# Optimization experiments

Hardware: AMD Instinct MI355X
Metric: run time of the kernel (lower is better)

## Reference

```python
import jax, jax.numpy as jnp
import numpy as np

# Config (mirrors init_kwargs)
B, S = 1, 2048          # batch, seq_len
H = 2048                # hidden_size
NH, NKV = 16, 8         # attention heads, kv heads (GQA n_rep = 2)
HD = H // NH            # head_dim = 128
I = 5632                # intermediate_size
L = 2                   # num_hidden_layers
V = 32000               # vocab_size
WIN = 1024              # sliding_window
THETA = 10000.0
EPS = 1e-6


def setup_inputs() -> dict:
    key = jax.random.key(0)
    ks = jax.random.split(key, 12)
    s = 0.02
    return {
        "input_ids": jax.random.randint(ks[0], (B, S), 0, V, dtype=jnp.int32),
        "embed": jax.random.normal(ks[1], (V, H), jnp.float32) * s,
        "Wq": jax.random.normal(ks[2], (L, H, NH * HD), jnp.float32) * s,
        "Wk": jax.random.normal(ks[3], (L, H, NKV * HD), jnp.float32) * s,
        "Wv": jax.random.normal(ks[4], (L, H, NKV * HD), jnp.float32) * s,
        "Wo": jax.random.normal(ks[5], (L, NH * HD, H), jnp.float32) * s,
        "Wg": jax.random.normal(ks[6], (L, H, I), jnp.float32) * s,
        "Wu": jax.random.normal(ks[7], (L, H, I), jnp.float32) * s,
        "Wd": jax.random.normal(ks[8], (L, I, H), jnp.float32) * s,
        "ln1": jnp.ones((L, H), jnp.float32),
        "ln2": jnp.ones((L, H), jnp.float32),
        "norm_w": jnp.ones((H,), jnp.float32),
    }


def _rmsnorm(x, w, eps=EPS):
    return x * jax.lax.rsqrt(jnp.mean(x * x, axis=-1, keepdims=True) + eps) * w


def _rope_tables(seq_len, dim, theta):
    inv_freq = 1.0 / (theta ** (jnp.arange(0, dim, 2, dtype=jnp.float32) / dim))
    freqs = jnp.arange(seq_len, dtype=jnp.float32)[:, None] * inv_freq[None, :]  # [S, dim/2]
    emb = jnp.concatenate([freqs, freqs], axis=-1)  # [S, dim]
    return jnp.cos(emb), jnp.sin(emb)


def _rotate_half(x):
    half = x.shape[-1] // 2
    return jnp.concatenate([-x[..., half:], x[..., :half]], axis=-1)


def _sliding_window_causal_mask(seq_len, window, dtype):
    i = jnp.arange(seq_len)[:, None]
    j = jnp.arange(seq_len)[None, :]
    allowed = (j <= i) & (j >= i - window)  # band: causal + sliding window
    return jnp.where(allowed, 0.0, jnp.finfo(dtype).min).astype(dtype)[None, None]  # [1,1,S,S]


def _forward(input_ids, embed, Wq, Wk, Wv, Wo, Wg, Wu, Wd, ln1, ln2, norm_w):
    x = embed[input_ids]  # [B,S,H]
    cos, sin = _rope_tables(S, HD, THETA)          # [S,HD]
    cos = cos[None, :, None, :]                    # [1,S,1,HD]
    sin = sin[None, :, None, :]
    mask = _sliding_window_causal_mask(S, WIN, x.dtype)  # [1,1,S,S]
    scale = 1.0 / jnp.sqrt(jnp.float32(HD)).astype(x.dtype)
    n_rep = NH // NKV

    for l in range(L):
        # --- attention block ---
        h = _rmsnorm(x, ln1[l])
        q = (h @ Wq[l]).reshape(B, S, NH, HD)
        k = (h @ Wk[l]).reshape(B, S, NKV, HD)
        v = (h @ Wv[l]).reshape(B, S, NKV, HD)
        q = q * cos + _rotate_half(q) * sin
        k = k * cos + _rotate_half(k) * sin
        # repeat_kv (GQA)
        k = jnp.broadcast_to(k[:, :, :, None, :], (B, S, NKV, n_rep, HD)).reshape(B, S, NH, HD)
        v = jnp.broadcast_to(v[:, :, :, None, :], (B, S, NKV, n_rep, HD)).reshape(B, S, NH, HD)
        scores = jnp.einsum('bshn,bthn->bhst', q, k) * scale + mask  # [B,NH,S,S]
        attn = jax.nn.softmax(scores.astype(jnp.float32), axis=-1).astype(x.dtype)
        o = jnp.einsum('bhst,bthn->bshn', attn, v).reshape(B, S, NH * HD)
        x = x + o @ Wo[l]
        # --- MLP block (SwiGLU) ---
        h = _rmsnorm(x, ln2[l])
        x = x + (jax.nn.silu(h @ Wg[l]) * (h @ Wu[l])) @ Wd[l]

    return _rmsnorm(x, norm_w)


def reference(input_ids, embed, Wq, Wk, Wv, Wo, Wg, Wu, Wd, ln1, ln2, norm_w):
    return _forward(input_ids, embed, Wq, Wk, Wv, Wo, Wg, Wu, Wd, ln1, ln2, norm_w)
```

## Files before the change

### kernel.cpp

```cpp
#include <hip/hip_runtime.h>
#include <stdint.h>

using bf16x8 = __attribute__((ext_vector_type(8))) __bf16;
using f32x4  = __attribute__((ext_vector_type(4))) float;

#define DEVI __device__ __forceinline__

DEVI unsigned short f2b(float f) {
  unsigned int u = __builtin_bit_cast(unsigned int, f);
  u = (u + 0x7FFFu + ((u >> 16) & 1u)) >> 16;
  return (unsigned short)u;
}
DEVI float b2f(unsigned short h) {
  unsigned int u = ((unsigned int)h) << 16;
  return __builtin_bit_cast(float, u);
}
DEVI f32x4 mfma16(bf16x8 a, bf16x8 b, f32x4 c) {
  return __builtin_amdgcn_mfma_f32_16x16x32_bf16(a, b, c, 0, 0, 0);
}
#define GLD(gp, lp) __builtin_amdgcn_global_load_lds( \
    (__attribute__((address_space(1))) void*)(uintptr_t)(gp), \
    (__attribute__((address_space(3))) void*)(uintptr_t)(lp), 16, 0, 0)

static constexpr int S_LEN = 2048;
static constexpr int HDIM  = 2048;
static constexpr int NH    = 16;
static constexpr int NKV   = 8;
static constexpr int HD    = 128;
static constexpr int IFF   = 5632;
static constexpr int WIN   = 1024;

DEVI void rms_finish(float4 v0, float4 v1, const float* __restrict__ w,
                     void* __restrict__ outp, int s, int t, int outf32) {
  float ss = v0.x*v0.x + v0.y*v0.y + v0.z*v0.z + v0.w*v0.w +
             v1.x*v1.x + v1.y*v1.y + v1.z*v1.z + v1.w*v1.w;
  #pragma unroll
  for (int off = 32; off >= 1; off >>= 1) ss += __shfl_xor(ss, off, 64);
  __shared__ float red[4];
  if ((t & 63) == 0) red[t >> 6] = ss;
  __syncthreads();
  ss = red[0] + red[1] + red[2] + red[3];
  float rr = rsqrtf(ss * (1.0f / 2048.0f) + 1e-6f);
  const float4* w4 = (const float4*)w;
  float4 w0 = w4[t], w1 = w4[t + 256];
  float o0x = v0.x*rr*w0.x, o0y = v0.y*rr*w0.y, o0z = v0.z*rr*w0.z, o0w = v0.w*rr*w0.w;
  float o1x = v1.x*rr*w1.x, o1y = v1.y*rr*w1.y, o1z = v1.z*rr*w1.z, o1w = v1.w*rr*w1.w;
  if (outf32) {
    float4* o4 = (float4*)outp + (size_t)s * 512;
    o4[t]       = make_float4(o0x, o0y, o0z, o0w);
    o4[t + 256] = make_float4(o1x, o1y, o1z, o1w);
  } else {
    uint2* ob = (uint2*)((unsigned short*)outp + (size_t)s * HDIM);
    ob[t]       = make_uint2((unsigned)f2b(o0x) | ((unsigned)f2b(o0y) << 16),
                             (unsigned)f2b(o0z) | ((unsigned)f2b(o0w) << 16));
    ob[t + 256] = make_uint2((unsigned)f2b(o1x) | ((unsigned)f2b(o1y) << 16),
                             (unsigned)f2b(o1z) | ((unsigned)f2b(o1w) << 16));
  }
}

__global__ __launch_bounds__(256) void gather_kernel(const int* __restrict__ ids,
    const float* __restrict__ embed, float* __restrict__ x,
    float* __restrict__ ct, float* __restrict__ st,
    const float* __restrict__ ln1w, unsigned short* __restrict__ h) {
  int s = blockIdx.x, t = threadIdx.x;
  const float4* src = (const float4*)(embed + (size_t)ids[s] * HDIM);
  float4* dst = (float4*)(x + (size_t)s * HDIM);
  float4 v0 = src[t], v1 = src[t + 256];
  dst[t]       = v0;
  dst[t + 256] = v1;
  if (t < 64) {
    float inv = expf(-(float)t * (9.210340371976184f / 64.0f));
    float f = (float)s * inv;
    ct[s * 64 + t] = cosf(f);
    st[s * 64 + t] = sinf(f);
  }
  rms_finish(v0, v1, ln1w, h, s, t, 0);
}

template<int OUTF32, int NPARTS>
__global__ __launch_bounds__(256) void rmsnorm_combine_kernel(
    float* __restrict__ x, const unsigned short* __restrict__ parts,
    const float* __restrict__ w, void* __restrict__ outp) {
  int s = blockIdx.x, t = threadIdx.x;
  const size_t PS = (size_t)2048 * 2048;
  float4* row = (float4*)(x + (size_t)s * HDIM);
  float4 v0 = row[t], v1 = row[t + 256];
  #pragma unroll
  for (int p = 0; p < NPARTS; ++p) {
    const unsigned short* pr = parts + p * PS + (size_t)s * HDIM;
    uint2 a = *(const uint2*)(pr + t * 4);
    uint2 b = *(const uint2*)(pr + (t + 256) * 4);
    v0.x += b2f((unsigned short)a.x); v0.y += b2f((unsigned short)(a.x >> 16));
    v0.z += b2f((unsigned short)a.y); v0.w += b2f((unsigned short)(a.y >> 16));
    v1.x += b2f((unsigned short)b.x); v1.y += b2f((unsigned short)(b.x >> 16));
    v1.z += b2f((unsigned short)b.y); v1.w += b2f((unsigned short)(b.y >> 16));
  }
  row[t] = v0; row[t + 256] = v1;
  rms_finish(v0, v1, w, outp, s, t, OUTF32);
}

__global__ __launch_bounds__(256) void convert_weights_kernel(
    const float* __restrict__ Wq, const float* __restrict__ Wk,
    const float* __restrict__ Wv, const float* __restrict__ Wo,
    const float* __restrict__ Wg, const float* __restrict__ Wu,
    const float* __restrict__ Wd,
    unsigned short* wqkvT, unsigned short* woT,
    unsigned short* wguT, unsigned short* wdT) {
  __shared__ float tl[128 * 65];
  int b = blockIdx.x;
  const float* in; unsigned short* out; int istr, ostr, tilesN, t; int guAdd = -1;
  if (b < 512)       { in = Wq; out = wqkvT;                       istr = 2048; ostr = 2048; tilesN = 32; t = b; }
  else if (b < 768)  { in = Wk; out = wqkvT + (size_t)2048 * 2048; istr = 1024; ostr = 2048; tilesN = 16; t = b - 512; }
  else if (b < 1024) { in = Wv; out = wqkvT + (size_t)3072 * 2048; istr = 1024; ostr = 2048; tilesN = 16; t = b - 768; }
  else if (b < 1536) { in = Wo; out = woT;                         istr = 2048; ostr = 2048; tilesN = 32; t = b - 1024; }
  else if (b < 2944) { in = Wg; out = wguT;                        istr = 5632; ostr = 2048; tilesN = 88; t = b - 1536; guAdd = 0; }
  else if (b < 4352) { in = Wu; out = wguT;                        istr = 5632; ostr = 2048; tilesN = 88; t = b - 2944; guAdd = 128; }
  else               { in = Wd; out = wdT;                         istr = 2048; ostr = 5632; tilesN = 32; t = b - 4352; }
  int k0 = (t / tilesN) * 128, n0 = (t % tilesN) * 64;
  int tx = threadIdx.x & 63, ty = threadIdx.x >> 6;
  #pragma unroll
  for (int i = 0; i < 32; ++i)
    tl[(ty + 4 * i) * 65 + tx] = in[(size_t)(k0 + ty + 4 * i) * istr + (n0 + tx)];
  __syncthreads();
  int ob = (guAdd >= 0) ? (((n0 >> 7) << 8) + (n0 & 64) + guAdd) : n0;
  unsigned int* ou = (unsigned int*)out;
  const int kstr2 = ostr >> 1;
  #pragma unroll
  for (int i = 0; i < 16; ++i) {
    int nrow = ty + 4 * i;
    float lo = tl[(2 * tx) * 65 + nrow], hi = tl[(2 * tx + 1) * 65 + nrow];
    ou[(size_t)(ob + nrow) * kstr2 + (k0 >> 1) + tx] =
        (unsigned int)f2b(lo) | ((unsigned int)f2b(hi) << 16);
  }
}

DEVI bf16x8 ldsAB(const unsigned short* buf, int r, int cbyte) {
  return *(const bf16x8*)((const unsigned char*)buf + r * 128 + (cbyte ^ ((r & 7) << 4)));
}
DEVI void stage_unit(const unsigned short* __restrict__ G, int Kstr,
                     unsigned short* lbuf, int loff0, int grow0,
                     int loff1, int grow1, int w, int l) {
  const int rsub = l >> 3;
  const int ce = ((l & 7) ^ rsub) << 3;
  const unsigned short* s0 = G + (size_t)(grow0 + w * 8 + rsub) * Kstr + ce;
  GLD(s0, (unsigned char*)lbuf + loff0 + w * 1024 + l * 16);
  const unsigned short* s1 = G + (size_t)(grow1 + w * 8 + rsub) * Kstr + ce;
  GLD(s1, (unsigned char*)lbuf + loff1 + w * 1024 + l * 16);
}
DEVI void stage128(const unsigned short* __restrict__ G, int Kstr,
                   unsigned short* slotbase, int h, int w, int l) {
  stage_unit(G, Kstr, slotbase, h * 16384, h * 128, h * 16384 + 8192, h * 128 + 64, w, l);
}

template<int Q>
DEVI void phase128(const unsigned short* Ab, f32x4 (&acc)[4][4],
                   bf16x8 (&breg)[2][4], int wr, int lg, int li) {
  const int r0 = wr * 64 + Q * 16 + li;
  bf16x8 a0 = ldsAB(Ab, r0, lg * 16);
  bf16x8 a1 = ldsAB(Ab, r0, 64 + lg * 16);
  __builtin_amdgcn_s_setprio(1);
  #pragma unroll
  for (int n = 0; n < 4; ++n) acc[Q][n] = mfma16(a0, breg[0][n], acc[Q][n]);
  #pragma unroll
  for (int n = 0; n < 4; ++n) acc[Q][n] = mfma16(a1, breg[1][n], acc[Q][n]);
  __builtin_amdgcn_s_setprio(0);
}

template<int EPI>
__global__ __launch_bounds__(512, 1) void gemm128_kernel(
    const unsigned short* __restrict__ A, const unsigned short* __restrict__ Bt,
    void* __restrict__ Cout, int Kstr, int nt, int parts, int nbm, int ldc,
    long long partStride,
    const float* __restrict__ ct, const float* __restrict__ st,
    unsigned short* __restrict__ ko, unsigned short* __restrict__ vt) {
  __shared__ __align__(16) unsigned char smem[131072];
  unsigned short* As0 = (unsigned short*)smem;
  unsigned short* Bs0 = (unsigned short*)(smem + 32768);
  const int tid = threadIdx.x, l = tid & 63, w = tid >> 6;
  const int lg = l >> 4, li = l & 15;
  const int wr = w >> 2, wc = w & 3;
  const int nb = gridDim.x, qx = nb >> 3;
  const int wg = ((int)blockIdx.x & 7) * qx + ((int)blockIdx.x >> 3);
  const int nbT = nb / parts;
  const int tile = wg % nbT, part = wg / nbT;
  const int m0 = (tile % nbm) * 128, n0 = (tile / nbm) * 256;
  const int kOff = part * (nt << 6);
  const unsigned short* At  = A  + (size_t)m0 * Kstr + kOff;
  const unsigned short* Bto = Bt + (size_t)n0 * Kstr + kOff;
  f32x4 acc[4][4] = {};
  bf16x8 breg[2][4];

  stage_unit(Bto, Kstr, Bs0, 0, 0, 8192, 64, w, l);
  stage_unit(Bto, Kstr, Bs0, 16384, 128, 24576, 192, w, l);
  stage_unit(At,  Kstr, As0, 0, 0, 8192, 64, w, l);
  { int k1 = (nt > 1) ? 64 : 0;
    stage_unit(Bto + k1, Kstr, Bs0 + 16384, 0, 0, 8192, 64, w, l);
    stage_unit(Bto + k1, Kstr, Bs0 + 16384, 16384, 128, 24576, 192, w, l); }
  asm volatile("s_waitcnt vmcnt(4)\n\ts_barrier" ::: "memory");

  for (int t = 0; t < nt; ++t) {
    unsigned short* Ab  = As0 + (t & 1) * 8192;
    unsigned short* Bb  = Bs0 + (t & 1) * 16384;
    unsigned short* Abn = As0 + ((t & 1) ^ 1) * 8192;
    const int kt1 = ((t + 1 < nt) ? t + 1 : nt - 1) << 6;
    const int kt2 = ((t + 2 < nt) ? t + 2 : nt - 1) << 6;
    stage_unit(At + kt1, Kstr, Abn, 0, 0, 8192, 64, w, l);
    #pragma unroll
    for (int ks = 0; ks < 2; ++ks)
      #pragma unroll
      for (int n = 0; n < 4; ++n)
        breg[ks][n] = ldsAB(Bb, wc * 64 + n * 16 + li, ks * 64 + lg * 16);
    asm volatile("s_waitcnt lgkmcnt(0)\n\ts_barrier" ::: "memory");
    phase128<0>(Ab, acc, breg, wr, lg, li);
    stage_unit(Bto + kt2, Kstr, Bb, 0, 0, 8192, 64, w, l);
    phase128<1>(Ab, acc, breg, wr, lg, li);
    stage_unit(Bto + kt2, Kstr, Bb, 16384, 128, 24576, 192, w, l);
    phase128<2>(Ab, acc, breg, wr, lg, li);
    phase128<3>(Ab, acc, breg, wr, lg, li);
    asm volatile("s_waitcnt vmcnt(4) lgkmcnt(0)\n\ts_barrier" ::: "memory");
  }
  asm volatile("s_waitcnt vmcnt(0)" ::: "memory");

  if (EPI == 0) {
    unsigned short* C = (unsigned short*)Cout + (size_t)part * (size_t)partStride;
    #pragma unroll
    for (int m = 0; m < 4; ++m)
      #pragma unroll
      for (int n = 0; n < 4; ++n) {
        int col = n0 + wc * 64 + n * 16 + li;
        #pragma unroll
        for (int r = 0; r < 4; ++r) {
          int row = m0 + wr * 64 + m * 16 + lg * 4 + r;
          C[(size_t)row * ldc + col] = f2b(acc[m][n][r]);
        }
      }
  } else {
    float* dump = (float*)smem;
    asm volatile("s_barrier" ::: "memory");
    #pragma unroll
    for (int m = 0; m < 4; ++m)
      #pragma unroll
      for (int n = 0; n < 4; ++n) {
        int colL = wc * 64 + n * 16 + li;
        #pragma unroll
        for (int r = 0; r < 4; ++r) {
          int rowl = wr * 64 + m * 16 + lg * 4 + r;
          dump[rowl * 256 + colL] = acc[m][n][r];
        }
      }
    asm volatile("s_waitcnt lgkmcnt(0)\n\ts_barrier" ::: "memory");
    if (n0 < 3072) {
      unsigned short* qk = (n0 < 2048) ? (unsigned short*)Cout : ko;
      const int cbase = (n0 < 2048) ? n0 : (n0 - 2048);
      const int ostr  = (n0 < 2048) ? 2048 : 1024;
      #pragma unroll
      for (int m = 0; m < 4; ++m)
        #pragma unroll
        for (int n = 0; n < 4; ++n) {
          int colL = wc * 64 + n * 16 + li;
          int hi = colL & 64;
          #pragma unroll
          for (int r = 0; r < 4; ++r) {
            int rowl = wr * 64 + m * 16 + lg * 4 + r;
            int s = m0 + rowl;
            float own = dump[rowl * 256 + colL];
            float par = dump[rowl * 256 + (colL ^ 64)];
            float c  = ct[s * 64 + (colL & 63)];
            float sn = st[s * 64 + (colL & 63)];
            float v = hi ? (own * c + par * sn) : (own * c - par * sn);
            qk[(size_t)s * ostr + cbase + colL] = f2b(v);
          }
        }
    } else {
      int vcol = tid >> 1, sh = (tid & 1) * 64;
      unsigned short* dstp = vt + (size_t)(n0 - 3072 + vcol) * 2048 + m0 + sh;
      #pragma unroll
      for (int c8 = 0; c8 < 8; ++c8) {
        unsigned short pk[8];
        #pragma unroll
        for (int i = 0; i < 8; ++i)
          pk[i] = f2b(dump[(sh + c8 * 8 + i) * 256 + vcol]);
        *(uint4*)(dstp + c8 * 8) = *(const uint4*)pk;
      }
    }
  }
}

template<int Q>
DEVI void ph256(const unsigned short* Ab, f32x4 (&acc)[8][4],
                bf16x8 (&breg)[2][4], int wr, int lg, int li) {
  bf16x8 a[2][2];
  #pragma unroll
  for (int mi = 0; mi < 2; ++mi)
    #pragma unroll
    for (int ks = 0; ks < 2; ++ks)
      a[mi][ks] = ldsAB(Ab, wr * 128 + Q * 32 + mi * 16 + li, ks * 64 + lg * 16);
  asm volatile("s_barrier" ::: "memory");
  asm volatile("s_waitcnt lgkmcnt(0)" ::: "memory");
  __builtin_amdgcn_sched_barrier(0);
  __builtin_amdgcn_s_setprio(1);
  #pragma unroll
  for (int mi = 0; mi < 2; ++mi)
    #pragma unroll
    for (int ks = 0; ks < 2; ++ks)
      #pragma unroll
      for (int n = 0; n < 4; ++n)
        acc[Q * 2 + mi][n] = mfma16(a[mi][ks], breg[ks][n], acc[Q * 2 + mi][n]);
  __builtin_amdgcn_s_setprio(0);
}

__global__ __launch_bounds__(512, 1) void gemm256p8_kernel(
    const unsigned short* __restrict__ A, const unsigned short* __restrict__ Bt,
    unsigned short* __restrict__ Cout, int Kstr, int nt, int nbm, int ldc) {
  __shared__ __align__(16) unsigned char smem[131072];
  unsigned short* As = (unsigned short*)smem;
  unsigned short* Bs = (unsigned short*)(smem + 65536);
  const int tid = threadIdx.x, l = tid & 63, w = tid >> 6;
  const int lg = l >> 4, li = l & 15;
  const int wr = w >> 2, wc = w & 3;
  const int nb = gridDim.x, qx = nb >> 3;
  const int wg = ((int)blockIdx.x & 7) * qx + ((int)blockIdx.x >> 3);
  const int m0 = (wg % nbm) * 256, n0 = (wg / nbm) * 256;
  const unsigned short* At  = A  + (size_t)m0 * Kstr;
  const unsigned short* Bto = Bt + (size_t)n0 * Kstr;
  unsigned short* A0 = As,  * A1 = As + 16384;
  unsigned short* B0 = Bs,  * B1 = Bs + 16384;
  f32x4 acc[8][4] = {};
  bf16x8 breg[2][4];

  stage128(At, Kstr, A0, 0, w, l);
  stage128(At, Kstr, A0, 1, w, l);
  stage128(Bto, Kstr, B0, 0, w, l);
  stage128(Bto, Kstr, B0, 1, w, l);
  stage128(Bto + 64, Kstr, B1, 0, w, l);
  stage128(Bto + 64, Kstr, B1, 1, w, l);
  asm volatile("s_waitcnt vmcnt(4)\n\ts_barrier" ::: "memory");

  const int nt2 = nt >> 1;
  for (int u = 0; u < nt2; ++u) {
    const int k1 = 2 * u + 1;
    const int k2 = (2 * u + 2 < nt) ? 2 * u + 2 : nt - 2;
    const int k3 = (2 * u + 3 < nt) ? 2 * u + 3 : nt - 1;
    #pragma unroll
    for (int ks = 0; ks < 2; ++ks)
      #pragma unroll
      for (int n = 0; n < 4; ++n)
        breg[ks][n] = ldsAB(B0, wc * 64 + n * 16 + li, ks * 64 + lg * 16);
    stage128(At + (k1 << 6), Kstr, A1, 0, w, l);
    ph256<0>(A0, acc, breg, wr, lg, li);
    asm volatile("s_barrier" ::: "memory");
    stage128(At + (k1 << 6), Kstr, A1, 1, w, l);
    ph256<1>(A0, acc, breg, wr, lg, li);
    asm volatile("s_barrier" ::: "memory");
    stage128(Bto + (k2 << 6), Kstr, B0, 0, w, l);
    ph256<2>(A0, acc, breg, wr, lg, li);
    asm volatile("s_barrier" ::: "memory");
    stage128(Bto + (k2 << 6), Kstr, B0, 1, w, l);
    ph256<3>(A0, acc, breg, wr, lg, li);
    asm volatile("s_waitcnt vmcnt(4)\n\ts_barrier" ::: "memory");
    #pragma unroll
    for (int ks = 0; ks < 2; ++ks)
      #pragma unroll
      for (int n = 0; n < 4; ++n)
        breg[ks][n] = ldsAB(B1, wc * 64 + n * 16 + li, ks * 64 + lg * 16);
    stage128(At + (k2 << 6), Kstr, A0, 0, w, l);
    ph256<0>(A1, acc, breg, wr, lg, li);
    asm volatile("s_barrier" ::: "memory");
    stage128(At + (k2 << 6), Kstr, A0, 1, w, l);
    ph256<1>(A1, acc, breg, wr, lg, li);
    asm volatile("s_barrier" ::: "memory");
    stage128(Bto + (k3 << 6), Kstr, B1, 0, w, l);
    ph256<2>(A1, acc, breg, wr, lg, li);
    asm volatile("s_barrier" ::: "memory");
    stage128(Bto + (k3 << 6), Kstr, B1, 1, w, l);
    ph256<3>(A1, acc, breg, wr, lg, li);
    asm volatile("s_waitcnt vmcnt(4)\n\ts_barrier" ::: "memory");
  }
  asm volatile("s_waitcnt vmcnt(0)" ::: "memory");

  float* ub = (float*)smem;
  asm volatile("s_barrier" ::: "memory");
  if (wc >= 2) {
    #pragma unroll
    for (int m = 0; m < 8; ++m)
      #pragma unroll
      for (int n = 0; n < 4; ++n) {
        int colL = (wc - 2) * 64 + n * 16 + li;
        #pragma unroll
        for (int r = 0; r < 4; ++r) {
          int rowl = wr * 128 + m * 16 + lg * 4 + r;
          ub[rowl * 128 + colL] = acc[m][n][r];
        }
      }
  }
  asm volatile("s_waitcnt lgkmcnt(0)\n\ts_barrier" ::: "memory");
  if (wc < 2) {
    const int col0 = n0 >> 1;
    #pragma unroll
    for (int m = 0; m < 8; ++m)
      #pragma unroll
      for (int n = 0; n < 4; ++n) {
        int colL = wc * 64 + n * 16 + li;
        #pragma unroll
        for (int r = 0; r < 4; ++r) {
          int rowl = wr * 128 + m * 16 + lg * 4 + r;
          float g = acc[m][n][r];
          float u = ub[rowl * 128 + colL];
          Cout[(size_t)(m0 + rowl) * ldc + col0 + colL] =
              f2b(g / (1.0f + __expf(-g)) * u);
        }
      }
  }
}

DEVI void stageKV(const unsigned short* __restrict__ kg,
                  const unsigned short* __restrict__ vtg, int kv, int j0,
                  unsigned short* Kbuf, unsigned short* Vbuf, int w, int l) {
  #pragma unroll
  for (int p = 0; p < 2; ++p) {
    int off = p * 8192 + w * 1024 + l * 16;
    int row = off >> 8;
    int colb = (off & 255) ^ ((row & 7) << 4);
    GLD(kg + (size_t)(j0 + row) * (NKV * HD) + kv * HD + (colb >> 1),
        (unsigned char*)Kbuf + off);
  }
  #pragma unroll
  for (int p = 0; p < 2; ++p) {
    int off = p * 8192 + w * 1024 + l * 16;
    int d = off >> 7;
    int colb = (off & 127) ^ ((d & 7) << 4);
    GLD(vtg + (size_t)(kv * HD + d) * S_LEN + j0 + (colb >> 1),
        (unsigned char*)Vbuf + off);
  }
}

__global__ __launch_bounds__(512) void attn_kernel(
    const unsigned short* __restrict__ qg, const unsigned short* __restrict__ kg,
    const unsigned short* __restrict__ vtg, unsigned short* __restrict__ og) {
  __shared__ __align__(16) unsigned short Kl[2][64 * 128];
  __shared__ __align__(16) unsigned short Vtl[2][128 * 64];
  __shared__ __align__(16) unsigned short Plds[8][16 * 72];
  const int tid = threadIdx.x, l = tid & 63, w = tid >> 6;
  const int lg = l >> 4, li = l & 15;
  const int i0 = blockIdx.x * 64, kv = blockIdx.y;
  const int hq = kv * 2 + (w >> 2);
  const int qr0 = i0 + (w & 3) * 16;
  const float scale = 0.08838834764831845f;

  bf16x8 qf[4];
  {
    const unsigned short* qrow = qg + (size_t)(qr0 + li) * (NH * HD) + hq * HD;
    #pragma unroll
    for (int sl = 0; sl < 4; ++sl)
      qf[sl] = *(const bf16x8*)(qrow + sl * 32 + lg * 8);
  }
  f32x4 oacc[8] = {};
  float mrow[4] = {-1e30f, -1e30f, -1e30f, -1e30f};
  float srow[4] = {0.f, 0.f, 0.f, 0.f};

  int jstart = i0 - WIN; if (jstart < 0) jstart = 0;
  stageKV(kg, vtg, kv, jstart, Kl[0], Vtl[0], w, l);

  int it = 0;
  for (int j0 = jstart; j0 <= i0; j0 += 64, ++it) {
    const int cur = it & 1;
    asm volatile("s_waitcnt vmcnt(0) lgkmcnt(0)\n\ts_barrier" ::: "memory");
    if (j0 + 64 <= i0)
      stageKV(kg, vtg, kv, j0 + 64, Kl[cur ^ 1], Vtl[cur ^ 1], w, l);
    const unsigned short* Klds  = Kl[cur];
    const unsigned short* Vtlds = Vtl[cur];

    f32x4 sacc[4] = {};
    #pragma unroll
    for (int nt = 0; nt < 4; ++nt) {
      int kr = nt * 16 + li;
      #pragma unroll
      for (int sl = 0; sl < 4; ++sl) {
        int cb = (sl * 64 + lg * 16) ^ ((kr & 7) << 4);
        bf16x8 kf = *(const bf16x8*)&Klds[(kr * 256 + cb) >> 1];
        sacc[nt] = mfma16(qf[sl], kf, sacc[nt]);
      }
    }

    float pv[4][4];
    #pragma unroll
    for (int r = 0; r < 4; ++r) {
      int qi = qr0 + lg * 4 + r;
      float sval[4];
      float tm = -1e30f;
      #pragma unroll
      for (int nt = 0; nt < 4; ++nt) {
        int j = j0 + nt * 16 + li;
        bool ok = (j <= qi) && (j + WIN >= qi);
        float sv = ok ? sacc[nt][r] * scale : -1e30f;
        sval[nt] = sv;
        tm = fmaxf(tm, sv);
      }
      #pragma unroll
      for (int off2 = 1; off2 < 16; off2 <<= 1)
        tm = fmaxf(tm, __shfl_xor(tm, off2, 64));
      float mnew = fmaxf(mrow[r], tm);
      float resc = __expf(mrow[r] - mnew);
      mrow[r] = mnew;
      float rs = 0.f;
      #pragma unroll
      for (int nt = 0; nt < 4; ++nt) {
        float p = (sval[nt] > -9e29f) ? __expf(sval[nt] - mnew) : 0.f;
        pv[nt][r] = p;
        rs += p;
      }
      #pragma unroll
      for (int off2 = 1; off2 < 16; off2 <<= 1)
        rs += __shfl_xor(rs, off2, 64);
      srow[r] = srow[r] * resc + rs;
      #pragma unroll
      for (int dt = 0; dt < 8; ++dt) oacc[dt][r] *= resc;
    }

    #pragma unroll
    for (int r = 0; r < 4; ++r)
      #pragma unroll
      for (int nt = 0; nt < 4; ++nt)
        Plds[w][(lg * 4 + r) * 72 + nt * 16 + li] = f2b(pv[nt][r]);
    bf16x8 ap[2];
    #pragma unroll
    for (int ks = 0; ks < 2; ++ks)
      ap[ks] = *(const bf16x8*)&Plds[w][li * 72 + ks * 32 + lg * 8];
    #pragma unroll
    for (int dt = 0; dt < 8; ++dt) {
      int d = dt * 16 + li;
      #pragma unroll
      for (int ks = 0; ks < 2; ++ks) {
        int cb = (ks * 64 + lg * 16) ^ ((d & 7) << 4);
        bf16x8 vf = *(const bf16x8*)&Vtlds[(d * 128 + cb) >> 1];
        oacc[dt] = mfma16(ap[ks], vf, oacc[dt]);
      }
    }
  }

  #pragma unroll
  for (int r = 0; r < 4; ++r) {
    float inv = 1.0f / srow[r];
    int qi = qr0 + lg * 4 + r;
    unsigned short* orow = og + (size_t)qi * (NH * HD) + hq * HD;
    #pragma unroll
    for (int dt = 0; dt < 8; ++dt)
      orow[dt * 16 + li] = f2b(oacc[dt][r] * inv);
  }
}

extern "C" void kernel_launch(void* const* d_in, const int* in_sizes, int n_in,
                              void* d_out, int out_size, void* d_ws, size_t ws_size,
                              hipStream_t stream) {
  const int*   ids   = (const int*)d_in[0];
  const float* embed = (const float*)d_in[1];
  const float* Wq    = (const float*)d_in[2];
  const float* Wk    = (const float*)d_in[3];
  const float* Wv    = (const float*)d_in[4];
  const float* Wo    = (const float*)d_in[5];
  const float* Wg    = (const float*)d_in[6];
  const float* Wu    = (const float*)d_in[7];
  const float* Wd    = (const float*)d_in[8];
  const float* ln1   = (const float*)d_in[9];
  const float* ln2   = (const float*)d_in[10];
  const float* normw = (const float*)d_in[11];

  uint8_t* ws = (uint8_t*)d_ws;
  unsigned short* wqkvT = (unsigned short*)(ws + 0);
  unsigned short* woT   = (unsigned short*)(ws + 16777216ull);
  unsigned short* wguT  = (unsigned short*)(ws + 25165824ull);
  unsigned short* wdT   = (unsigned short*)(ws + 71303168ull);
  float*          x     = (float*)(ws + 94371840ull);
  unsigned short* h     = (unsigned short*)(ws + 111149056ull);
  unsigned short* q     = (unsigned short*)(ws + 119537664ull);
  unsigned short* k     = (unsigned short*)(ws + 127926272ull);
  unsigned short* vt    = (unsigned short*)(ws + 132120576ull);
  unsigned short* o     = (unsigned short*)(ws + 136314880ull);
  unsigned short* act   = (unsigned short*)(ws + 119537664ull);
  unsigned short* pbuf  = (unsigned short*)(ws + 144703488ull);
  float*          cost  = (float*)(ws + 213909504ull);
  float*          sint  = (float*)(ws + 214433792ull);
  const long long PSel = 4194304LL;

  gather_kernel<<<2048, 256, 0, stream>>>(ids, embed, x, cost, sint, ln1, h);

  for (int l = 0; l < 2; ++l) {
    convert_weights_kernel<<<5760, 256, 0, stream>>>(
        Wq + (size_t)l * 2048 * 2048, Wk + (size_t)l * 2048 * 1024,
        Wv + (size_t)l * 2048 * 1024, Wo + (size_t)l * 2048 * 2048,
        Wg + (size_t)l * 2048 * 5632, Wu + (size_t)l * 2048 * 5632,
        Wd + (size_t)l * 5632 * 2048,
        wqkvT, woT, wguT, wdT);
    if (l == 1)
      rmsnorm_combine_kernel<0, 2><<<2048, 256, 0, stream>>>(x, pbuf, ln1 + 2048, h);
    gemm128_kernel<4><<<256, 512, 0, stream>>>(h, wqkvT, q, 2048, 32, 1, 16, 2048, 0,
                                               cost, sint, k, vt);
    attn_kernel<<<dim3(32, 8), 512, 0, stream>>>(q, k, vt, o);
    gemm128_kernel<0><<<256, 512, 0, stream>>>(o, woT, pbuf, 2048, 16, 2, 16, 2048, PSel,
                                               nullptr, nullptr, nullptr, nullptr);
    rmsnorm_combine_kernel<0, 2><<<2048, 256, 0, stream>>>(x, pbuf, ln2 + l * 2048, h);
    gemm256p8_kernel<<<352, 512, 0, stream>>>(h, wguT, act, 2048, 32, 8, 5632);
    gemm128_kernel<0><<<256, 512, 0, stream>>>(act, wdT, pbuf, 5632, 44, 2, 16, 2048, PSel,
                                               nullptr, nullptr, nullptr, nullptr);
  }
  rmsnorm_combine_kernel<1, 2><<<2048, 256, 0, stream>>>(x, pbuf, normw, d_out);
  (void)in_sizes; (void)n_in; (void)out_size; (void)ws_size;
}
```

Before: 688.7 us.

## Triple-buffer B in gemm128, swap GEMM kernels per stage, add lazy softmax rescale

The 128-tile GEMM now triple-buffers its B operand, which removes a barrier per k-iteration. It also gains a SwiGLU epilogue and now handles the gate/up projection with 704 blocks. The 256x256 kernel becomes a split-K kernel with 4 parts and is used for the Wo and Wd projections, so rmsnorm_combine sums 4 partial buffers. Attention skips the max reduction and rescale when the new block max exceeds the running max by no more than 8. This rebalances tile sizes and occupancy per GEMM, at the cost of more partial-sum traffic and possible precision drift from the deferred rescale.

```diff
diff --git a/kernel.cpp b/kernel.cpp
--- a/kernel.cpp
+++ b/kernel.cpp
@@ -189,18 +189,20 @@
   const unsigned short* Bto = Bt + (size_t)n0 * Kstr + kOff;
   f32x4 acc[4][4] = {};
   bf16x8 breg[2][4];
-
-  stage_unit(Bto, Kstr, Bs0, 0, 0, 8192, 64, w, l);
-  stage_unit(Bto, Kstr, Bs0, 16384, 128, 24576, 192, w, l);
+  unsigned short* B0p = Bs0;
+  unsigned short* B1p = Bs0 + 16384;
+  unsigned short* B2p = Bs0 + 32768;
+
+  stage_unit(Bto, Kstr, B0p, 0, 0, 8192, 64, w, l);
+  stage_unit(Bto, Kstr, B0p, 16384, 128, 24576, 192, w, l);
   stage_unit(At,  Kstr, As0, 0, 0, 8192, 64, w, l);
   { int k1 = (nt > 1) ? 64 : 0;
-    stage_unit(Bto + k1, Kstr, Bs0 + 16384, 0, 0, 8192, 64, w, l);
-    stage_unit(Bto + k1, Kstr, Bs0 + 16384, 16384, 128, 24576, 192, w, l); }
+    stage_unit(Bto + k1, Kstr, B1p, 0, 0, 8192, 64, w, l);
+    stage_unit(Bto + k1, Kstr, B1p, 16384, 128, 24576, 192, w, l); }
   asm volatile("s_waitcnt vmcnt(4)\n\ts_barrier" ::: "memory");
 
   for (int t = 0; t < nt; ++t) {
     unsigned short* Ab  = As0 + (t & 1) * 8192;
-    unsigned short* Bb  = Bs0 + (t & 1) * 16384;
     unsigned short* Abn = As0 + ((t & 1) ^ 1) * 8192;
     const int kt1 = ((t + 1 < nt) ? t + 1 : nt - 1) << 6;
     const int kt2 = ((t + 2 < nt) ? t + 2 : nt - 1) << 6;
@@ -209,15 +211,15 @@
     for (int ks = 0; ks < 2; ++ks)
       #pragma unroll
       for (int n = 0; n < 4; ++n)
-        breg[ks][n] = ldsAB(Bb, wc * 64 + n * 16 + li, ks * 64 + lg * 16);
-    asm volatile("s_waitcnt lgkmcnt(0)\n\ts_barrier" ::: "memory");
+        breg[ks][n] = ldsAB(B0p, wc * 64 + n * 16 + li, ks * 64 + lg * 16);
     phase128<0>(Ab, acc, breg, wr, lg, li);
-    stage_unit(Bto + kt2, Kstr, Bb, 0, 0, 8192, 64, w, l);
+    stage_unit(Bto + kt2, Kstr, B2p, 0, 0, 8192, 64, w, l);
     phase128<1>(Ab, acc, breg, wr, lg, li);
-    stage_unit(Bto + kt2, Kstr, Bb, 16384, 128, 24576, 192, w, l);
+    stage_unit(Bto + kt2, Kstr, B2p, 16384, 128, 24576, 192, w, l);
     phase128<2>(Ab, acc, breg, wr, lg, li);
     phase128<3>(Ab, acc, breg, wr, lg, li);
     asm volatile("s_waitcnt vmcnt(4) lgkmcnt(0)\n\ts_barrier" ::: "memory");
+    unsigned short* tmp = B0p; B0p = B1p; B1p = B2p; B2p = tmp;
   }
   asm volatile("s_waitcnt vmcnt(0)" ::: "memory");
 
@@ -234,6 +236,41 @@
           C[(size_t)row * ldc + col] = f2b(acc[m][n][r]);
         }
       }
+  } else if (EPI == 3) {
+    float* ub = (float*)smem;
+    asm volatile("s_barrier" ::: "memory");
+    if (wc >= 2) {
+      #pragma unroll
+      for (int m = 0; m < 4; ++m)
+        #pragma unroll
+        for (int n = 0; n < 4; ++n) {
+          int colL = (wc - 2) * 64 + n * 16 + li;
+          #pragma unroll
+          for (int r = 0; r < 4; ++r) {
+            int rowl = wr * 64 + m * 16 + lg * 4 + r;
+            ub[rowl * 128 + colL] = acc[m][n][r];
+          }
+        }
+    }
+    asm volatile("s_waitcnt lgkmcnt(0)\n\ts_barrier" ::: "memory");
+    if (wc < 2) {
+      unsigned short* act = (unsigned short*)Cout;
+      const int col0 = n0 >> 1;
+      #pragma unroll
+      for (int m = 0; m < 4; ++m)
+        #pragma unroll
+        for (int n = 0; n < 4; ++n) {
+          int colL = wc * 64 + n * 16 + li;
+          #pragma unroll
+          for (int r = 0; r < 4; ++r) {
+            int rowl = wr * 64 + m * 16 + lg * 4 + r;
+            float g = acc[m][n][r];
+            float u = ub[rowl * 128 + colL];
+            act[(size_t)(m0 + rowl) * ldc + col0 + colL] =
+                f2b(g / (1.0f + __expf(-g)) * u);
+          }
+        }
+    }
   } else {
     float* dump = (float*)smem;
     asm volatile("s_barrier" ::: "memory");
@@ -311,7 +348,8 @@
 
 __global__ __launch_bounds__(512, 1) void gemm256p8_kernel(
     const unsigned short* __restrict__ A, const unsigned short* __restrict__ Bt,
-    unsigned short* __restrict__ Cout, int Kstr, int nt, int nbm, int ldc) {
+    unsigned short* __restrict__ Cout, int Kstr, int nt, int parts, int nbm,
+    int ldc, long long partStride) {
   __shared__ __align__(16) unsigned char smem[131072];
   unsigned short* As = (unsigned short*)smem;
   unsigned short* Bs = (unsigned short*)(smem + 65536);
@@ -320,9 +358,12 @@
   const int wr = w >> 2, wc = w & 3;
   const int nb = gridDim.x, qx = nb >> 3;
   const int wg = ((int)blockIdx.x & 7) * qx + ((int)blockIdx.x >> 3);
-  const int m0 = (wg % nbm) * 256, n0 = (wg / nbm) * 256;
-  const unsigned short* At  = A  + (size_t)m0 * Kstr;
-  const unsigned short* Bto = Bt + (size_t)n0 * Kstr;
+  const int nbT = nb / parts;
+  const int tile = wg % nbT, part = wg / nbT;
+  const int m0 = (tile % nbm) * 256, n0 = (tile / nbm) * 256;
+  const int kOff = part * (nt << 6);
+  const unsigned short* At  = A  + (size_t)m0 * Kstr + kOff;
+  const unsigned short* Bto = Bt + (size_t)n0 * Kstr + kOff;
   unsigned short* A0 = As,  * A1 = As + 16384;
   unsigned short* B0 = Bs,  * B1 = Bs + 16384;
   f32x4 acc[8][4] = {};
@@ -378,39 +419,18 @@
   }
   asm volatile("s_waitcnt vmcnt(0)" ::: "memory");
 
-  float* ub = (float*)smem;
-  asm volatile("s_barrier" ::: "memory");
-  if (wc >= 2) {
-    #pragma unroll
-    for (int m = 0; m < 8; ++m)
-      #pragma unroll
-      for (int n = 0; n < 4; ++n) {
-        int colL = (wc - 2) * 64 + n * 16 + li;
-        #pragma unroll
-        for (int r = 0; r < 4; ++r) {
-          int rowl = wr * 128 + m * 16 + lg * 4 + r;
-          ub[rowl * 128 + colL] = acc[m][n][r];
-        }
-      }
-  }
-  asm volatile("s_waitcnt lgkmcnt(0)\n\ts_barrier" ::: "memory");
-  if (wc < 2) {
-    const int col0 = n0 >> 1;
-    #pragma unroll
-    for (int m = 0; m < 8; ++m)
-      #pragma unroll
-      for (int n = 0; n < 4; ++n) {
-        int colL = wc * 64 + n * 16 + li;
-        #pragma unroll
-        for (int r = 0; r < 4; ++r) {
-          int rowl = wr * 128 + m * 16 + lg * 4 + r;
-          float g = acc[m][n][r];
-          float u = ub[rowl * 128 + colL];
-          Cout[(size_t)(m0 + rowl) * ldc + col0 + colL] =
-              f2b(g / (1.0f + __expf(-g)) * u);
-        }
-      }
-  }
+  unsigned short* C = Cout + (size_t)part * (size_t)partStride;
+  #pragma unroll
+  for (int m = 0; m < 8; ++m)
+    #pragma unroll
+    for (int n = 0; n < 4; ++n) {
+      int col = n0 + wc * 64 + n * 16 + li;
+      #pragma unroll
+      for (int r = 0; r < 4; ++r) {
+        int row = m0 + wr * 128 + m * 16 + lg * 4 + r;
+        C[(size_t)row * ldc + col] = f2b(acc[m][n][r]);
+      }
+    }
 }
 
 DEVI void stageKV(const unsigned short* __restrict__ kg,
@@ -483,38 +503,62 @@
     }
 
     float pv[4][4];
+    float sval[4][4], pmax[4];
     #pragma unroll
     for (int r = 0; r < 4; ++r) {
       int qi = qr0 + lg * 4 + r;
-      float sval[4];
       float tm = -1e30f;
       #pragma unroll
       for (int nt = 0; nt < 4; ++nt) {
         int j = j0 + nt * 16 + li;
         bool ok = (j <= qi) && (j + WIN >= qi);
         float sv = ok ? sacc[nt][r] * scale : -1e30f;
-        sval[nt] = sv;
+        sval[r][nt] = sv;
         tm = fmaxf(tm, sv);
       }
-      #pragma unroll
-      for (int off2 = 1; off2 < 16; off2 <<= 1)
-        tm = fmaxf(tm, __shfl_xor(tm, off2, 64));
-      float mnew = fmaxf(mrow[r], tm);
-      float resc = __expf(mrow[r] - mnew);
-      mrow[r] = mnew;
-      float rs = 0.f;
-      #pragma unroll
-      for (int nt = 0; nt < 4; ++nt) {
-        float p = (sval[nt] > -9e29f) ? __expf(sval[nt] - mnew) : 0.f;
-        pv[nt][r] = p;
-        rs += p;
-      }
-      #pragma unroll
-      for (int off2 = 1; off2 < 16; off2 <<= 1)
-        rs += __shfl_xor(rs, off2, 64);
-      srow[r] = srow[r] * resc + rs;
-      #pragma unroll
-      for (int dt = 0; dt < 8; ++dt) oacc[dt][r] *= resc;
+      pmax[r] = tm;
+    }
+    bool cond = (pmax[0] - mrow[0] <= 8.f) && (pmax[1] - mrow[1] <= 8.f) &&
+                (pmax[2] - mrow[2] <= 8.f) && (pmax[3] - mrow[3] <= 8.f);
+    if (__all(cond)) {
+      #pragma unroll
+      for (int r = 0; r < 4; ++r) {
+        float rs = 0.f;
+        #pragma unroll
+        for (int nt = 0; nt < 4; ++nt) {
+          float p = (sval[r][nt] > -9e29f) ? __expf(sval[r][nt] - mrow[r]) : 0.f;
+          pv[nt][r] = p;
+          rs += p;
+        }
+        #pragma unroll
+        for (int off2 = 1; off2 < 16; off2 <<= 1)
+          rs += __shfl_xor(rs, off2, 64);
+        srow[r] += rs;
+      }
+    } else {
+      #pragma unroll
+      for (int r = 0; r < 4; ++r) {
+        float tm = pmax[r];
+        #pragma unroll
+        for (int off2 = 1; off2 < 16; off2 <<= 1)
+          tm = fmaxf(tm, __shfl_xor(tm, off2, 64));
+        float mnew = fmaxf(mrow[r], tm);
+        float resc = __expf(mrow[r] - mnew);
+        mrow[r] = mnew;
+        float rs = 0.f;
+        #pragma unroll
+        for (int nt = 0; nt < 4; ++nt) {
+          float p = (sval[r][nt] > -9e29f) ? __expf(sval[r][nt] - mnew) : 0.f;
+          pv[nt][r] = p;
+          rs += p;
+        }
+        #pragma unroll
+        for (int off2 = 1; off2 < 16; off2 <<= 1)
+          rs += __shfl_xor(rs, off2, 64);
+        srow[r] = srow[r] * resc + rs;
+        #pragma unroll
+        for (int dt = 0; dt < 8; ++dt) oacc[dt][r] *= resc;
+      }
     }
 
     #pragma unroll
@@ -592,17 +636,16 @@
         Wd + (size_t)l * 5632 * 2048,
         wqkvT, woT, wguT, wdT);
     if (l == 1)
-      rmsnorm_combine_kernel<0, 2><<<2048, 256, 0, stream>>>(x, pbuf, ln1 + 2048, h);
+      rmsnorm_combine_kernel<0, 4><<<2048, 256, 0, stream>>>(x, pbuf, ln1 + 2048, h);
     gemm128_kernel<4><<<256, 512, 0, stream>>>(h, wqkvT, q, 2048, 32, 1, 16, 2048, 0,
                                                cost, sint, k, vt);
     attn_kernel<<<dim3(32, 8), 512, 0, stream>>>(q, k, vt, o);
-    gemm128_kernel<0><<<256, 512, 0, stream>>>(o, woT, pbuf, 2048, 16, 2, 16, 2048, PSel,
+    gemm256p8_kernel<<<256, 512, 0, stream>>>(o, woT, pbuf, 2048, 8, 4, 8, 2048, PSel);
+    rmsnorm_combine_kernel<0, 4><<<2048, 256, 0, stream>>>(x, pbuf, ln2 + l * 2048, h);
+    gemm128_kernel<3><<<704, 512, 0, stream>>>(h, wguT, act, 2048, 32, 1, 16, 5632, 0,
                                                nullptr, nullptr, nullptr, nullptr);
-    rmsnorm_combine_kernel<0, 2><<<2048, 256, 0, stream>>>(x, pbuf, ln2 + l * 2048, h);
-    gemm256p8_kernel<<<352, 512, 0, stream>>>(h, wguT, act, 2048, 32, 8, 5632);
-    gemm128_kernel<0><<<256, 512, 0, stream>>>(act, wdT, pbuf, 5632, 44, 2, 16, 2048, PSel,
-                                               nullptr, nullptr, nullptr, nullptr);
-  }
-  rmsnorm_combine_kernel<1, 2><<<2048, 256, 0, stream>>>(x, pbuf, normw, d_out);
+    gemm256p8_kernel<<<256, 512, 0, stream>>>(act, wdT, pbuf, 5632, 22, 4, 8, 2048, PSel);
+  }
+  rmsnorm_combine_kernel<1, 4><<<2048, 256, 0, stream>>>(x, pbuf, normw, d_out);
   (void)in_sizes; (void)n_in; (void)out_size; (void)ws_size;
 }
```

New measurement: 669.1 us. -2.9%, faster.
